# Kernel tuning notes

Hardware: AMD Instinct MI355X
Metric: run time of the kernel (lower is better)

The kernel has to match this reference:

```python
import jax, jax.numpy as jnp
import numpy as np

N, D, C, R, O = 256, 64, 32, 16, 32  # batch, features, in-channels (left=right), repetitions, out-channels


def setup_inputs() -> dict:
    key = jax.random.key(0)
    k1, k2, k3 = jax.random.split(key, 3)
    left_ll = jax.random.normal(k1, (N, D, C, R), dtype=jnp.float32)
    right_ll = jax.random.normal(k2, (N, D, C, R), dtype=jnp.float32)
    logits = jax.random.normal(k3, (D, O, R, C, C), dtype=jnp.float32)
    return {"left_ll": left_ll, "right_ll": right_ll, "logits": logits}


def reference(left_ll, right_ll, logits):
    # Normalized weights: softmax over flattened (i, j) channel-pair axis.
    f, co, r, i, j = logits.shape
    weights = jax.nn.softmax(logits.reshape(f, co, r, i * j), axis=-1).reshape(f, co, r, i, j)

    # LogEinsumExp trick: subtract per-(feature, rep) channel max, exponentiate,
    # contract in linear space, then return to log space.
    left_max = jnp.max(left_ll, axis=2, keepdims=True)    # (N, D, 1, R)
    right_max = jnp.max(right_ll, axis=2, keepdims=True)  # (N, D, 1, R)
    left_prob = jnp.exp(left_ll - left_max)
    right_prob = jnp.exp(right_ll - right_max)

    # (N, D, O, R) weighted cross-product over left/right channels.
    prob = jnp.einsum('ndir,ndjr,dorij->ndor', left_prob, right_prob, weights)
    return jnp.log(prob) + left_max + right_max  # maxes broadcast over out-channel axis
```

## Files before the change

### kernel.cpp

```cpp
#include <hip/hip_runtime.h>

#define N_ 256
#define D_ 64
#define C_ 32
#define R_ 16
#define O_ 32

typedef _Float16 half8 __attribute__((ext_vector_type(8)));
typedef float f32x16 __attribute__((ext_vector_type(16)));

__global__ __launch_bounds__(256) void prep_kernel(
    const float* __restrict__ left, const float* __restrict__ right,
    _Float16* __restrict__ lw, _Float16* __restrict__ rw,
    float* __restrict__ msum) {
  const int b = blockIdx.x, t = threadIdx.x;
  const int n = ((b >> 3) << 1) | (t >> 7);
  const int d = ((b & 7) << 3) | ((t >> 4) & 7);
  const int r = t & 15;
  const size_t sbase = ((size_t)(n * D_ + d) * C_) * R_ + r;
  const size_t dbase = (size_t)((d * R_ + r) * N_ + n) * C_;

  float lmx = -1e30f, rmx = -1e30f;
  {
    float vals[C_];
#pragma unroll
    for (int i = 0; i < C_; i++) {
      float v = left[sbase + (size_t)i * R_];
      vals[i] = v;
      lmx = fmaxf(lmx, v);
    }
    half8 pk[4];
#pragma unroll
    for (int i = 0; i < C_; i++) pk[i >> 3][i & 7] = (_Float16)__expf(vals[i] - lmx);
    half8* dst = (half8*)(lw + dbase);
#pragma unroll
    for (int q = 0; q < 4; q++) dst[q] = pk[q];
  }
  {
    float vals[C_];
#pragma unroll
    for (int i = 0; i < C_; i++) {
      float v = right[sbase + (size_t)i * R_];
      vals[i] = v;
      rmx = fmaxf(rmx, v);
    }
    half8 pk[4];
#pragma unroll
    for (int i = 0; i < C_; i++) pk[i >> 3][i & 7] = (_Float16)__expf(vals[i] - rmx);
    half8* dst = (half8*)(rw + dbase);
#pragma unroll
    for (int q = 0; q < 4; q++) dst[q] = pk[q];
  }
  msum[(d * R_ + r) * N_ + n] = lmx + rmx;
}

__global__ __launch_bounds__(512, 4) void main_kernel(
    const float* __restrict__ logits, const _Float16* __restrict__ lw,
    const _Float16* __restrict__ rw, const float* __restrict__ msum,
    float* __restrict__ out) {
  __shared__ _Float16 Wl[32 * 64 * 8];
  __shared__ float psum[16][32];
  __shared__ float msum_s[N_];

  const int bid = blockIdx.x;
  const int workid = ((bid & 7) << 7) | (bid >> 3);
  const int d = workid >> 4, r = workid & 15;

  const int t = threadIdx.x;
  const int w = t >> 6, l = t & 63;
  const int o = l & 31, jb = l >> 5;

  const _Float16* lbase = lw + (size_t)((d * R_ + r) * N_) * C_;
  const _Float16* rbase = rw + (size_t)((d * R_ + r) * N_) * C_;
  const int row = (w << 5) | o;
  const half8* lp = (const half8*)(lbase + row * C_ + (jb << 4));
  const half8 LhA = lp[0];
  const half8 LhB = lp[1];
  const half8* rp2 = (const half8*)(rbase + row * C_);
  half8 Rh[4];
#pragma unroll
  for (int q = 0; q < 4; q++) Rh[q] = rp2[q];

  if (t < N_) msum_s[t] = msum[(d * R_ + r) * N_ + t];

  const int o_a = t & 31, ih = t >> 5;
  const float* lgrow =
      logits + ((size_t)((d * O_ + o_a) * R_ + r) * C_) * C_;
  const int i0 = ((ih >> 3) << 4) | (ih & 7);
  const int slot = ((ih >> 3) << 5) | o_a;
  const int sbase_a = (ih & 7) << 2;

  float lsum = 0.f;

  float4 v0[8];
  {
    const float4* rp = (const float4*)(lgrow + i0 * C_);
#pragma unroll
    for (int q = 0; q < 8; q++) v0[q] = rp[q];
  }
#pragma unroll
  for (int q2 = 0; q2 < 4; q2++) {
    half8 hh;
    float tmp[8] = {v0[q2 * 2].x,     v0[q2 * 2].y,     v0[q2 * 2].z,
                    v0[q2 * 2].w,     v0[q2 * 2 + 1].x, v0[q2 * 2 + 1].y,
                    v0[q2 * 2 + 1].z, v0[q2 * 2 + 1].w};
#pragma unroll
    for (int p = 0; p < 8; p++) {
      float e = __expf(tmp[p]);
      lsum += e;
      hh[p] = (_Float16)e;
    }
    *(half8*)&Wl[(((sbase_a | q2) << 6) | slot) << 3] = hh;
  }
  __syncthreads();

  float4 v1[8];
  {
    const float4* rp = (const float4*)(lgrow + (i0 + 8) * C_);
#pragma unroll
    for (int q = 0; q < 8; q++) v1[q] = rp[q];
  }

  f32x16 acc;
#pragma unroll
  for (int g = 0; g < 16; g++) acc[g] = 0.f;

#pragma unroll
  for (int s = 0; s < 32; s++) {
    const half8 Bf = *(const half8*)&Wl[((s << 6) | l) << 3];
    const _Float16 Lsc = LhA[s >> 2];
    const half8 Ld = {Lsc, Lsc, Lsc, Lsc, Lsc, Lsc, Lsc, Lsc};
    acc = __builtin_amdgcn_mfma_f32_32x32x16_f16(Ld * Rh[s & 3], Bf, acc, 0, 0, 0);
  }
  __syncthreads();

#pragma unroll
  for (int q2 = 0; q2 < 4; q2++) {
    half8 hh;
    float tmp[8] = {v1[q2 * 2].x,     v1[q2 * 2].y,     v1[q2 * 2].z,
                    v1[q2 * 2].w,     v1[q2 * 2 + 1].x, v1[q2 * 2 + 1].y,
                    v1[q2 * 2 + 1].z, v1[q2 * 2 + 1].w};
#pragma unroll
    for (int p = 0; p < 8; p++) {
      float e = __expf(tmp[p]);
      lsum += e;
      hh[p] = (_Float16)e;
    }
    *(half8*)&Wl[(((sbase_a | q2) << 6) | slot) << 3] = hh;
  }
  psum[ih][o_a] = lsum;
  __syncthreads();

#pragma unroll
  for (int s = 0; s < 32; s++) {
    const half8 Bf = *(const half8*)&Wl[((s << 6) | l) << 3];
    const _Float16 Lsc = LhB[s >> 2];
    const half8 Ld = {Lsc, Lsc, Lsc, Lsc, Lsc, Lsc, Lsc, Lsc};
    acc = __builtin_amdgcn_mfma_f32_32x32x16_f16(Ld * Rh[s & 3], Bf, acc, 0, 0, 0);
  }

  float tot = 0.f;
#pragma unroll
  for (int k = 0; k < 16; k++) tot += psum[k][o];
  const float rlogsum = __logf(tot);

#pragma unroll
  for (int g = 0; g < 16; g++) {
    const int n = (w << 5) | ((g & 3) + ((g >> 2) << 3) + (jb << 2));
    const float val = __logf(acc[g]) - rlogsum + msum_s[n];
    out[(((size_t)n * D_ + d) * O_ + o) * R_ + r] = val;
  }
}

extern "C" void kernel_launch(void* const* d_in, const int* in_sizes, int n_in,
                              void* d_out, int out_size, void* d_ws, size_t ws_size,
                              hipStream_t stream) {
  const float* left = (const float*)d_in[0];
  const float* right = (const float*)d_in[1];
  const float* logits = (const float*)d_in[2];
  float* out = (float*)d_out;
  _Float16* lw = (_Float16*)d_ws;
  _Float16* rw = (_Float16*)((char*)d_ws + (size_t)16 * 1024 * 1024);
  float* ms = (float*)((char*)d_ws + (size_t)32 * 1024 * 1024);

  prep_kernel<<<1024, 256, 0, stream>>>(left, right, lw, rw, ms);
  main_kernel<<<1024, 512, 0, stream>>>(logits, lw, rw, ms, out);
}
```

Measured before the change: 303.0 us.

## Coalesce logits loads, single-pass weight staging, and add transpose kernel for output

The main kernel now loads each logits row with fully coalesced float4 reads and stages all 64 K-slices of exp-weights into a doubled, XOR-swizzled LDS buffer in one pass. The softmax denominator is reduced with wavefront shuffles, which removes the second sync phase. Output is no longer scattered with stride-R writes. It goes to scratch buffers that alias the left/right workspace, and a new transpose kernel then writes the final layout coalesced through shared memory. The cost is an extra kernel launch, an extra round trip to global memory, and double the LDS use, which may lower occupancy.

```diff
diff --git a/kernel.cpp b/kernel.cpp
--- a/kernel.cpp
+++ b/kernel.cpp
@@ -7,6 +7,7 @@
 #define O_ 32
 
 typedef _Float16 half8 __attribute__((ext_vector_type(8)));
+typedef _Float16 half4 __attribute__((ext_vector_type(4)));
 typedef float f32x16 __attribute__((ext_vector_type(16)));
 
 __global__ __launch_bounds__(256) void prep_kernel(
@@ -55,11 +56,10 @@
 }
 
 __global__ __launch_bounds__(512, 4) void main_kernel(
-    const float* __restrict__ logits, const _Float16* __restrict__ lw,
-    const _Float16* __restrict__ rw, const float* __restrict__ msum,
-    float* __restrict__ out) {
-  __shared__ _Float16 Wl[32 * 64 * 8];
-  __shared__ float psum[16][32];
+    const float* __restrict__ logits, const _Float16* lw, const _Float16* rw,
+    const float* __restrict__ msum, float* scrA, float* scrB) {
+  __shared__ __align__(16) _Float16 Wl[64 * 64 * 8];
+  __shared__ float psum_o[32];
   __shared__ float msum_s[N_];
 
   const int bid = blockIdx.x;
@@ -83,92 +83,109 @@
 
   if (t < N_) msum_s[t] = msum[(d * R_ + r) * N_ + t];
 
-  const int o_a = t & 31, ih = t >> 5;
-  const float* lgrow =
-      logits + ((size_t)((d * O_ + o_a) * R_ + r) * C_) * C_;
-  const int i0 = ((ih >> 3) << 4) | (ih & 7);
-  const int slot = ((ih >> 3) << 5) | o_a;
-  const int sbase_a = (ih & 7) << 2;
-
-  float lsum = 0.f;
-
-  float4 v0[8];
-  {
-    const float4* rp = (const float4*)(lgrow + i0 * C_);
-#pragma unroll
-    for (int q = 0; q < 8; q++) v0[q] = rp[q];
-  }
-#pragma unroll
-  for (int q2 = 0; q2 < 4; q2++) {
-    half8 hh;
-    float tmp[8] = {v0[q2 * 2].x,     v0[q2 * 2].y,     v0[q2 * 2].z,
-                    v0[q2 * 2].w,     v0[q2 * 2 + 1].x, v0[q2 * 2 + 1].y,
-                    v0[q2 * 2 + 1].z, v0[q2 * 2 + 1].w};
-#pragma unroll
-    for (int p = 0; p < 8; p++) {
-      float e = __expf(tmp[p]);
-      lsum += e;
-      hh[p] = (_Float16)e;
-    }
-    *(half8*)&Wl[(((sbase_a | q2) << 6) | slot) << 3] = hh;
+  float lsum[4] = {0.f, 0.f, 0.f, 0.f};
+#pragma unroll
+  for (int hp = 0; hp < 2; hp++) {
+    float4 v[2][4];
+#pragma unroll
+    for (int sp = 0; sp < 2; sp++) {
+      const int sl = (hp << 1) | sp;
+      const int oa = (w << 2) | sl;
+      const float4* lg4 =
+          (const float4*)(logits + ((size_t)((d * O_ + oa) * R_ + r) << 10));
+#pragma unroll
+      for (int k = 0; k < 4; k++) v[sp][k] = lg4[(k << 6) + l];
+    }
+#pragma unroll
+    for (int sp = 0; sp < 2; sp++) {
+      const int sl = (hp << 1) | sp;
+      const int oa = (w << 2) | sl;
+#pragma unroll
+      for (int k = 0; k < 4; k++) {
+        const float4 f = v[sp][k];
+        const float e0 = __expf(f.x), e1 = __expf(f.y), e2 = __expf(f.z),
+                    e3 = __expf(f.w);
+        lsum[sl] += (e0 + e1) + (e2 + e3);
+        half4 hq = {(_Float16)e0, (_Float16)e1, (_Float16)e2, (_Float16)e3};
+        const int s_ = ((((k & 1) << 3) | (l >> 3)) << 2) | ((l & 7) >> 1);
+        const int slot_ = ((k >> 1) << 5) | oa;
+        const int byte_ =
+            ((s_ << 10) | (slot_ << 4) | ((l & 1) << 3)) ^ ((s_ & 7) << 4);
+        *(half4*)((char*)Wl + byte_) = hq;
+      }
+    }
+  }
+#pragma unroll
+  for (int sl = 0; sl < 4; sl++) {
+    float ss = lsum[sl];
+#pragma unroll
+    for (int off = 32; off >= 1; off >>= 1) ss += __shfl_xor(ss, off);
+    if (l == 0) psum_o[(w << 2) | sl] = ss;
   }
   __syncthreads();
 
-  float4 v1[8];
-  {
-    const float4* rp = (const float4*)(lgrow + (i0 + 8) * C_);
-#pragma unroll
-    for (int q = 0; q < 8; q++) v1[q] = rp[q];
-  }
+  const float rlogsum = __logf(psum_o[o]);
 
   f32x16 acc;
 #pragma unroll
   for (int g = 0; g < 16; g++) acc[g] = 0.f;
 
 #pragma unroll
-  for (int s = 0; s < 32; s++) {
-    const half8 Bf = *(const half8*)&Wl[((s << 6) | l) << 3];
-    const _Float16 Lsc = LhA[s >> 2];
+  for (int s = 0; s < 64; s++) {
+    const int byte_r = ((s << 10) | (l << 4)) ^ ((s & 7) << 4);
+    const half8 Bf = *(const half8*)((const char*)Wl + byte_r);
+    const int ig = s >> 2;
+    const _Float16 Lsc = (ig < 8) ? LhA[ig & 7] : LhB[ig & 7];
     const half8 Ld = {Lsc, Lsc, Lsc, Lsc, Lsc, Lsc, Lsc, Lsc};
     acc = __builtin_amdgcn_mfma_f32_32x32x16_f16(Ld * Rh[s & 3], Bf, acc, 0, 0, 0);
   }
+
+  float* sb = ((w < 4) ? scrA : scrB) + ((size_t)(d * R_ + r) << 12) +
+              (((w & 3) << 5) << 5) + o;
+#pragma unroll
+  for (int g = 0; g < 16; g++) {
+    const int rowt = (g & 3) + ((g >> 2) << 3) + (jb << 2);
+    const int n = (w << 5) | rowt;
+    const float val = __logf(acc[g]) - rlogsum + msum_s[n];
+    sb[rowt << 5] = val;
+  }
+}
+
+__global__ __launch_bounds__(256) void trans_kernel(const float* scrA,
+                                                    const float* scrB,
+                                                    float* __restrict__ out) {
+  __shared__ float tile[8 * 32 * 20];
+  const int bid = blockIdx.x;
+  const int d = bid >> 5, chunk = bid & 31;
+  const int n0 = chunk << 3;
+  const float* src = (chunk < 16) ? scrA : scrB;
+  const int t = threadIdx.x;
+
+  {
+    const int r_t = t >> 4, i16 = t & 15;
+    const float* rb =
+        src + ((size_t)(d * R_ + r_t) << 12) + (((chunk & 15) << 3) << 5);
+#pragma unroll
+    for (int k = 0; k < 4; k++) {
+      const int f = (k << 4) | i16;
+      const float4 v = *(const float4*)(rb + (f << 2));
+      const int nl = f >> 3, o4 = (f & 7) << 2;
+#pragma unroll
+      for (int j = 0; j < 4; j++)
+        tile[((nl << 5) | (o4 + j)) * 20 + r_t] = v[j];
+    }
+  }
   __syncthreads();
-
-#pragma unroll
-  for (int q2 = 0; q2 < 4; q2++) {
-    half8 hh;
-    float tmp[8] = {v1[q2 * 2].x,     v1[q2 * 2].y,     v1[q2 * 2].z,
-                    v1[q2 * 2].w,     v1[q2 * 2 + 1].x, v1[q2 * 2 + 1].y,
-                    v1[q2 * 2 + 1].z, v1[q2 * 2 + 1].w};
-#pragma unroll
-    for (int p = 0; p < 8; p++) {
-      float e = __expf(tmp[p]);
-      lsum += e;
-      hh[p] = (_Float16)e;
-    }
-    *(half8*)&Wl[(((sbase_a | q2) << 6) | slot) << 3] = hh;
-  }
-  psum[ih][o_a] = lsum;
-  __syncthreads();
-
-#pragma unroll
-  for (int s = 0; s < 32; s++) {
-    const half8 Bf = *(const half8*)&Wl[((s << 6) | l) << 3];
-    const _Float16 Lsc = LhB[s >> 2];
-    const half8 Ld = {Lsc, Lsc, Lsc, Lsc, Lsc, Lsc, Lsc, Lsc};
-    acc = __builtin_amdgcn_mfma_f32_32x32x16_f16(Ld * Rh[s & 3], Bf, acc, 0, 0, 0);
-  }
-
-  float tot = 0.f;
-#pragma unroll
-  for (int k = 0; k < 16; k++) tot += psum[k][o];
-  const float rlogsum = __logf(tot);
-
-#pragma unroll
-  for (int g = 0; g < 16; g++) {
-    const int n = (w << 5) | ((g & 3) + ((g >> 2) << 3) + (jb << 2));
-    const float val = __logf(acc[g]) - rlogsum + msum_s[n];
-    out[(((size_t)n * D_ + d) * O_ + o) * R_ + r] = val;
+  {
+    const int n_w = t >> 5, pos = t & 31;
+    float* ob = out + (((size_t)(n0 + n_w) * D_ + d) << 9);
+#pragma unroll
+    for (int k = 0; k < 4; k++) {
+      const int idx = (k << 5) | pos;
+      const float4 v =
+          *(const float4*)&tile[((n_w << 5) | (idx >> 2)) * 20 + ((pos & 3) << 2)];
+      *(float4*)(ob + (idx << 2)) = v;
+    }
   }
 }
 
@@ -182,7 +199,10 @@
   _Float16* lw = (_Float16*)d_ws;
   _Float16* rw = (_Float16*)((char*)d_ws + (size_t)16 * 1024 * 1024);
   float* ms = (float*)((char*)d_ws + (size_t)32 * 1024 * 1024);
+  float* scrA = (float*)d_ws;
+  float* scrB = (float*)((char*)d_ws + (size_t)16 * 1024 * 1024);
 
   prep_kernel<<<1024, 256, 0, stream>>>(left, right, lw, rw, ms);
-  main_kernel<<<1024, 512, 0, stream>>>(logits, lw, rw, ms, out);
-}
+  main_kernel<<<1024, 512, 0, stream>>>(logits, lw, rw, ms, scrA, scrB);
+  trans_kernel<<<2048, 256, 0, stream>>>(scrA, scrB, out);
+}
```

After: 275.6 us. 9.1% less time.
